# Kernel tuning notes

Hardware: AMD Instinct MI355X
Metric: run time of the kernel (lower is better)

Reference implementation:

```python
import jax, jax.numpy as jnp
import numpy as np

B, N, D, H = 8, 8192, 512, 8  # batch, seq, hidden, heads
DH = D // H


def _rope_tables(n, d, dtype=jnp.float32):
    # standard rotate-half RoPE tables over the full hidden dim (d/2 freq pairs)
    half = d // 2
    inv_freq = 1.0 / (10000.0 ** (np.arange(0, half, dtype=np.float32) / half))
    pos = np.arange(n, dtype=np.float32)
    ang = np.einsum('n,f->nf', pos, inv_freq)          # [N, D/2]
    ang = np.concatenate([ang, ang], axis=-1)          # [N, D]
    return jnp.asarray(np.cos(ang), dtype), jnp.asarray(np.sin(ang), dtype)


def setup_inputs() -> dict:
    key = jax.random.key(0)
    k1, k2 = jax.random.split(key)
    hidden_states = jax.random.normal(k1, (B, N, D), dtype=jnp.float32)
    num_layers = 24
    std = 0.02 / np.sqrt(2.0 * num_layers * D)
    W = jax.random.normal(k2, (D, D), dtype=jnp.float32) * std
    cos, sin = _rope_tables(N, D)
    return {"hidden_states": hidden_states, "W": W, "cos": cos, "sin": sin}


def _rotate_half(x):
    x1, x2 = jnp.split(x, 2, axis=-1)
    return jnp.concatenate([-x2, x1], axis=-1)


def reference(hidden_states, W, cos, sin):
    # dropout(p=0) in eval mode -> identity
    x = hidden_states * cos + _rotate_half(hidden_states) * sin  # RoPE, [B,N,D]
    q = jnp.einsum('bnd,ed->bne', x, W)                          # F.linear(x, W)
    qh = q.reshape(B, N, H, DH)
    xh = x.reshape(B, N, H, DH)
    # linear-complexity path: (K^T V) then Q @ (.), per head
    kv = jnp.einsum('bnhd,bnhe->bhde', xh, xh)   # [B,H,DH,DH]
    out = jnp.einsum('bnhd,bhde->bnhe', qh, kv)  # [B,N,H,DH]
    return out.reshape(B, N, D)
```

## Files before the change

### kernel.cpp

```cpp
#include <hip/hip_runtime.h>
#include <hip/hip_bf16.h>
#include <stdint.h>

#define BB 8
#define NN 8192
#define DD 512
#define HH 8
#define DHD 64
#define NCH 16

typedef __attribute__((ext_vector_type(8))) short bf16x8;
typedef __attribute__((ext_vector_type(4))) float f32x4;
typedef __attribute__((ext_vector_type(4))) float f4v;

__device__ __forceinline__ unsigned short f2bf(float f) {
  union { float f; unsigned int u; } v; v.f = f;
  return (unsigned short)((v.u + 0x7FFFu + ((v.u >> 16) & 1u)) >> 16);
}

__device__ __forceinline__ void async16(const void* g, void* l) {
  __builtin_amdgcn_global_load_lds(
      (const __attribute__((address_space(1))) void*)g,
      (__attribute__((address_space(3))) void*)l, 16, 0, 0);
}

__global__ void rope_kernel(const float* __restrict__ h, const float* __restrict__ cs,
                            const float* __restrict__ sn, unsigned short* __restrict__ x) {
  int t = blockIdx.x * 256 + threadIdx.x;
  int r = t >> 6;
  int c = (t & 63) << 2;
  int n = r & (NN - 1);
  size_t base  = (size_t)r * DD + c;
  size_t tbase = (size_t)n * DD + c;
  f4v h1 = __builtin_nontemporal_load((const f4v*)(h + base));
  f4v h2 = __builtin_nontemporal_load((const f4v*)(h + base + 256));
  f4v c1 = *(const f4v*)(cs + tbase);
  f4v c2 = *(const f4v*)(cs + tbase + 256);
  f4v s1 = *(const f4v*)(sn + tbase);
  f4v s2 = *(const f4v*)(sn + tbase + 256);
  f4v x1 = h1 * c1 - h2 * s1;
  f4v x2 = h2 * c2 + h1 * s2;
  uint2 p1, p2;
  p1.x = (unsigned)f2bf(x1.x) | ((unsigned)f2bf(x1.y) << 16);
  p1.y = (unsigned)f2bf(x1.z) | ((unsigned)f2bf(x1.w) << 16);
  p2.x = (unsigned)f2bf(x2.x) | ((unsigned)f2bf(x2.y) << 16);
  p2.y = (unsigned)f2bf(x2.z) | ((unsigned)f2bf(x2.w) << 16);
  *(uint2*)(x + base)       = p1;
  *(uint2*)(x + base + 256) = p2;
}

__global__ void kv_kernel(const unsigned short* __restrict__ x, float* __restrict__ kvp) {
  __shared__ __align__(16) unsigned short xt[64 * 68];
  int bh = blockIdx.x;
  int b = bh >> 3, hh = bh & 7;
  int chunk = blockIdx.y;
  int tid = threadIdx.x;
  int wave = tid >> 6, lane = tid & 63;
  int d0 = (wave & 1) * 32, e0 = (wave >> 1) * 32;
  int l15 = lane & 15, q = lane >> 4;
  f32x4 acc[2][2];
#pragma unroll
  for (int i = 0; i < 2; ++i)
#pragma unroll
    for (int j = 0; j < 2; ++j) acc[i][j] = (f32x4){0.f, 0.f, 0.f, 0.f};

  int rp  = tid & 31;
  int seg = tid >> 5;
  const unsigned short* srcbase = x + (size_t)b * NN * DD + hh * DHD + seg * 8;

  for (int t = 0; t < 8; ++t) {
    int n0 = chunk * 512 + t * 64;
    const unsigned short* s0 = srcbase + (size_t)(n0 + 2 * rp) * DD;
    uint4 p0 = *(const uint4*)(s0);
    uint4 p1 = *(const uint4*)(s0 + DD);
    unsigned short a0[8], a1[8];
    *(uint4*)a0 = p0;  *(uint4*)a1 = p1;
    __syncthreads();
#pragma unroll
    for (int j = 0; j < 8; ++j) {
      unsigned pack = (unsigned)a0[j] | ((unsigned)a1[j] << 16);
      ((unsigned*)xt)[(seg * 8 + j) * 34 + rp] = pack;
    }
    __syncthreads();
#pragma unroll
    for (int ks = 0; ks < 64; ks += 32) {
      bf16x8 a0f = *(const bf16x8*)&xt[(d0 + l15) * 68 + ks + q * 8];
      bf16x8 a1f = *(const bf16x8*)&xt[(d0 + 16 + l15) * 68 + ks + q * 8];
      bf16x8 b0f = *(const bf16x8*)&xt[(e0 + l15) * 68 + ks + q * 8];
      bf16x8 b1f = *(const bf16x8*)&xt[(e0 + 16 + l15) * 68 + ks + q * 8];
      acc[0][0] = __builtin_amdgcn_mfma_f32_16x16x32_bf16(a0f, b0f, acc[0][0], 0, 0, 0);
      acc[1][0] = __builtin_amdgcn_mfma_f32_16x16x32_bf16(a1f, b0f, acc[1][0], 0, 0, 0);
      acc[0][1] = __builtin_amdgcn_mfma_f32_16x16x32_bf16(a0f, b1f, acc[0][1], 0, 0, 0);
      acc[1][1] = __builtin_amdgcn_mfma_f32_16x16x32_bf16(a1f, b1f, acc[1][1], 0, 0, 0);
    }
  }
  float* dst = kvp + ((size_t)chunk * gridDim.x + bh) * 4096;
#pragma unroll
  for (int i = 0; i < 2; ++i)
#pragma unroll
    for (int j = 0; j < 2; ++j) {
      int col = e0 + j * 16 + l15;
#pragma unroll
      for (int reg = 0; reg < 4; ++reg) {
        int row = d0 + i * 16 + q * 4 + reg;
        dst[row * 64 + col] = acc[i][j][reg];
      }
    }
}

__global__ void wkvt_kernel(const float* __restrict__ W, const float* __restrict__ kvp,
                            unsigned short* __restrict__ wkvt) {
  __shared__ float kvs[4096];
  __shared__ float ws[8192];
  int bh = blockIdx.x, fc = blockIdx.y;
  int nbh = gridDim.x;
  int b = bh >> 3, hh = bh & 7;
  int f0 = fc * 128;
  int tid = threadIdx.x;
#pragma unroll
  for (int i = 0; i < 4; ++i) {
    int idx = i * 1024 + tid * 4;
    f4v s = (f4v){0.f, 0.f, 0.f, 0.f};
    for (int c = 0; c < NCH; ++c)
      s += *(const f4v*)&kvp[((size_t)c * nbh + bh) * 4096 + idx];
    *(f4v*)&kvs[idx] = s;
  }
#pragma unroll
  for (int i = 0; i < 8; ++i) {
    int idx = i * 1024 + tid * 4;
    int d = idx >> 7, f = idx & 127;
    *(float4*)&ws[idx] = *(const float4*)&W[(size_t)(hh * DHD + d) * DD + f0 + f];
  }
  __syncthreads();
  int e = tid & 63, fg = tid >> 6;
  float acc[32];
#pragma unroll
  for (int j = 0; j < 32; ++j) acc[j] = 0.f;
  for (int d = 0; d < 64; ++d) {
    float kvv = kvs[d * 64 + e];
    const float* wr = &ws[d * 128 + fg * 32];
#pragma unroll
    for (int j = 0; j < 32; ++j) acc[j] = fmaf(wr[j], kvv, acc[j]);
  }
  unsigned short tmp[32];
#pragma unroll
  for (int j = 0; j < 32; ++j) tmp[j] = f2bf(acc[j]);
  size_t obase = ((size_t)(b * DD + hh * DHD + e)) * DD + f0 + fg * 32;
#pragma unroll
  for (int qq = 0; qq < 4; ++qq)
    *(uint4*)&wkvt[obase + qq * 8] = *(uint4*)&tmp[qq * 8];
}

__global__ __launch_bounds__(256, 2) void gemm_kernel(const unsigned short* __restrict__ x,
                                                      const unsigned short* __restrict__ wkvt,
                                                      float* __restrict__ out) {
  __shared__ __align__(16) unsigned short As[128 * 64];
  __shared__ __align__(16) unsigned short Bs[256 * 64];
  int mt = blockIdx.x, ct = blockIdx.y, bz = blockIdx.z;
  int tid = threadIdx.x, wave = tid >> 6, lane = tid & 63;
  int m_off = (wave & 1) * 64, c_off = (wave >> 1) * 128;
  int l15 = lane & 15, q = lane >> 4;
  int lrow = lane >> 3, lcol = (lane & 7) * 8;
  const unsigned short* Ag = x    + ((size_t)bz * NN + mt * 128) * DD;
  const unsigned short* Bg = wkvt + ((size_t)bz * DD + ct * 256) * DD;
  f32x4 acc[4][8];
#pragma unroll
  for (int i = 0; i < 4; ++i)
#pragma unroll
    for (int j = 0; j < 8; ++j) acc[i][j] = (f32x4){0.f, 0.f, 0.f, 0.f};

  for (int kk = 0; kk < 512; kk += 64) {
#pragma unroll
    for (int i = 0; i < 4; ++i)
      async16(Ag + (size_t)(wave * 32 + i * 8 + lrow) * DD + kk + lcol,
              &As[(wave * 32 + i * 8) * 64]);
#pragma unroll
    for (int i = 0; i < 8; ++i)
      async16(Bg + (size_t)(wave * 64 + i * 8 + lrow) * DD + kk + lcol,
              &Bs[(wave * 64 + i * 8) * 64]);
    __syncthreads();
#pragma unroll
    for (int ks = 0; ks < 64; ks += 32) {
      bf16x8 a[4], bb[8];
#pragma unroll
      for (int i = 0; i < 4; ++i)
        a[i] = *(const bf16x8*)&As[(m_off + i * 16 + l15) * 64 + ks + q * 8];
#pragma unroll
      for (int j = 0; j < 8; ++j)
        bb[j] = *(const bf16x8*)&Bs[(c_off + j * 16 + l15) * 64 + ks + q * 8];
#pragma unroll
      for (int i = 0; i < 4; ++i)
#pragma unroll
        for (int j = 0; j < 8; ++j)
          acc[i][j] = __builtin_amdgcn_mfma_f32_16x16x32_bf16(a[i], bb[j], acc[i][j], 0, 0, 0);
    }
    __syncthreads();
  }
  float* ob = out + ((size_t)bz * NN + mt * 128) * DD + ct * 256;
#pragma unroll
  for (int i = 0; i < 4; ++i)
#pragma unroll
    for (int j = 0; j < 8; ++j) {
      int row = m_off + i * 16 + q * 4;
      int col = c_off + j * 16 + l15;
#pragma unroll
      for (int reg = 0; reg < 4; ++reg)
        ob[(size_t)(row + reg) * DD + col] = acc[i][j][reg];
    }
}

extern "C" void kernel_launch(void* const* d_in, const int* in_sizes, int n_in,
                              void* d_out, int out_size, void* d_ws, size_t ws_size,
                              hipStream_t stream) {
  (void)in_sizes; (void)n_in; (void)out_size;
  const float* h  = (const float*)d_in[0];
  const float* W  = (const float*)d_in[1];
  const float* cs = (const float*)d_in[2];
  const float* sn = (const float*)d_in[3];
  float* out = (float*)d_out;

  const size_t x_full     = (size_t)BB * NN * DD * 2;
  const size_t kvp_full   = (size_t)NCH * BB * HH * DHD * DHD * 4;
  const size_t wkvt_full  = (size_t)BB * DD * DD * 2;
  const size_t x_batch    = (size_t)NN * DD * 2;
  const size_t kvp_batch  = (size_t)NCH * HH * DHD * DHD * 4;
  const size_t wkvt_batch = (size_t)DD * DD * 2;

  if (ws_size >= x_full + kvp_full + wkvt_full) {
    unsigned short* xw   = (unsigned short*)d_ws;
    float*          kvp  = (float*)((char*)d_ws + x_full);
    unsigned short* wkvt = (unsigned short*)((char*)d_ws + x_full + kvp_full);
    rope_kernel<<<dim3(BB * NN * 64 / 256), dim3(256), 0, stream>>>(h, cs, sn, xw);
    kv_kernel<<<dim3(BB * HH, NCH), dim3(256), 0, stream>>>(xw, kvp);
    wkvt_kernel<<<dim3(BB * HH, 4), dim3(256), 0, stream>>>(W, kvp, wkvt);
    gemm_kernel<<<dim3(NN / 128, DD / 256, BB), dim3(256), 0, stream>>>(xw, wkvt, out);
  } else {
    unsigned short* xw   = (unsigned short*)d_ws;
    float*          kvp  = (float*)((char*)d_ws + x_batch);
    unsigned short* wkvt = (unsigned short*)((char*)d_ws + x_batch + kvp_batch);
    for (int b = 0; b < BB; ++b) {
      rope_kernel<<<dim3(NN * 64 / 256), dim3(256), 0, stream>>>(
          h + (size_t)b * NN * DD, cs, sn, xw);
      kv_kernel<<<dim3(HH, NCH), dim3(256), 0, stream>>>(xw, kvp);
      wkvt_kernel<<<dim3(HH, 4), dim3(256), 0, stream>>>(W, kvp, wkvt);
      gemm_kernel<<<dim3(NN / 128, DD / 256, 1), dim3(256), 0, stream>>>(
          xw, wkvt, out + (size_t)b * NN * DD);
    }
  }
}
```

Before: 335.4 us.

## Fuse RoPE into KV reduction kernel and restructure W·KV product

Merges the RoPE kernel with the per-head K^T V accumulation: each 512-thread block applies RoPE to 256 rows, writes the bf16 x for the later GEMM, and transposes the result into LDS to compute all 8 heads' 64x64 KV partials with MFMA, prefetching the next tile's inputs. This removes the separate launch and the re-read of x from global memory. The wkvt kernel is reshaped to load all of W's head rows per block with vectorized FMAs over 16 output columns, and the GEMM output uses nontemporal stores. The trade-off is only 256 blocks for the fused kernel, which may underfill the GPU, and more partial chunks to reduce.

```diff
diff --git a/kernel.cpp b/kernel.cpp
--- a/kernel.cpp
+++ b/kernel.cpp
@@ -7,7 +7,7 @@
 #define DD 512
 #define HH 8
 #define DHD 64
-#define NCH 16
+#define NCH 32
 
 typedef __attribute__((ext_vector_type(8))) short bf16x8;
 typedef __attribute__((ext_vector_type(4))) float f32x4;
@@ -24,131 +24,170 @@
       (__attribute__((address_space(3))) void*)l, 16, 0, 0);
 }
 
-__global__ void rope_kernel(const float* __restrict__ h, const float* __restrict__ cs,
-                            const float* __restrict__ sn, unsigned short* __restrict__ x) {
-  int t = blockIdx.x * 256 + threadIdx.x;
-  int r = t >> 6;
-  int c = (t & 63) << 2;
-  int n = r & (NN - 1);
-  size_t base  = (size_t)r * DD + c;
-  size_t tbase = (size_t)n * DD + c;
-  f4v h1 = __builtin_nontemporal_load((const f4v*)(h + base));
-  f4v h2 = __builtin_nontemporal_load((const f4v*)(h + base + 256));
-  f4v c1 = *(const f4v*)(cs + tbase);
-  f4v c2 = *(const f4v*)(cs + tbase + 256);
-  f4v s1 = *(const f4v*)(sn + tbase);
-  f4v s2 = *(const f4v*)(sn + tbase + 256);
-  f4v x1 = h1 * c1 - h2 * s1;
-  f4v x2 = h2 * c2 + h1 * s2;
-  uint2 p1, p2;
-  p1.x = (unsigned)f2bf(x1.x) | ((unsigned)f2bf(x1.y) << 16);
-  p1.y = (unsigned)f2bf(x1.z) | ((unsigned)f2bf(x1.w) << 16);
-  p2.x = (unsigned)f2bf(x2.x) | ((unsigned)f2bf(x2.y) << 16);
-  p2.y = (unsigned)f2bf(x2.z) | ((unsigned)f2bf(x2.w) << 16);
-  *(uint2*)(x + base)       = p1;
-  *(uint2*)(x + base + 256) = p2;
-}
-
-__global__ void kv_kernel(const unsigned short* __restrict__ x, float* __restrict__ kvp) {
-  __shared__ __align__(16) unsigned short xt[64 * 68];
-  int bh = blockIdx.x;
-  int b = bh >> 3, hh = bh & 7;
-  int chunk = blockIdx.y;
+__global__ __launch_bounds__(512, 2) void ropekv_kernel(
+    const float* __restrict__ h, const float* __restrict__ cs,
+    const float* __restrict__ sn, unsigned short* __restrict__ x,
+    float* __restrict__ kvp, int nbh) {
+  __shared__ __align__(16) unsigned int xt32[512 * 34];
+  int blk = blockIdx.x;
+  int chunk = blk & 31, b = blk >> 5;
   int tid = threadIdx.x;
   int wave = tid >> 6, lane = tid & 63;
-  int d0 = (wave & 1) * 32, e0 = (wave >> 1) * 32;
+  int rpar = lane & 1;
+  int g = lane >> 1;
+  int cf = g * 8;
   int l15 = lane & 15, q = lane >> 4;
-  f32x4 acc[2][2];
-#pragma unroll
-  for (int i = 0; i < 2; ++i)
-#pragma unroll
-    for (int j = 0; j < 2; ++j) acc[i][j] = (f32x4){0.f, 0.f, 0.f, 0.f};
-
-  int rp  = tid & 31;
-  int seg = tid >> 5;
-  const unsigned short* srcbase = x + (size_t)b * NN * DD + hh * DHD + seg * 8;
-
-  for (int t = 0; t < 8; ++t) {
-    int n0 = chunk * 512 + t * 64;
-    const unsigned short* s0 = srcbase + (size_t)(n0 + 2 * rp) * DD;
-    uint4 p0 = *(const uint4*)(s0);
-    uint4 p1 = *(const uint4*)(s0 + DD);
-    unsigned short a0[8], a1[8];
-    *(uint4*)a0 = p0;  *(uint4*)a1 = p1;
-    __syncthreads();
-#pragma unroll
-    for (int j = 0; j < 8; ++j) {
-      unsigned pack = (unsigned)a0[j] | ((unsigned)a1[j] << 16);
-      ((unsigned*)xt)[(seg * 8 + j) * 34 + rp] = pack;
-    }
-    __syncthreads();
+  int hd = wave * 64;
+  size_t row0 = (size_t)b * NN + (size_t)chunk * 256;
+  int n0 = chunk * 256;
+
+  f32x4 acc[4][4];
+#pragma unroll
+  for (int i = 0; i < 4; ++i)
+#pragma unroll
+    for (int j = 0; j < 4; ++j) acc[i][j] = (f32x4){0.f, 0.f, 0.f, 0.f};
+
+  f4v ha[4][2], hbv[4][2];
+
+  auto loadt = [&](int t) {
+#pragma unroll
+    for (int p = 0; p < 4; ++p) {
+      int r = p * 16 + wave * 2 + rpar;
+      const float* hp = h + (row0 + t * 64 + r) * DD + cf;
+      ha[p][0]  = __builtin_nontemporal_load((const f4v*)hp);
+      ha[p][1]  = __builtin_nontemporal_load((const f4v*)(hp + 4));
+      hbv[p][0] = __builtin_nontemporal_load((const f4v*)(hp + 256));
+      hbv[p][1] = __builtin_nontemporal_load((const f4v*)(hp + 260));
+    }
+  };
+
+  auto ropet = [&](int t) {
+#pragma unroll
+    for (int p = 0; p < 4; ++p) {
+      int r = p * 16 + wave * 2 + rpar;
+      int nr = n0 + t * 64 + r;
+      const float* cp = cs + (size_t)nr * DD + cf;
+      const float* sp = sn + (size_t)nr * DD + cf;
+      f4v c0 = *(const f4v*)cp, c1 = *(const f4v*)(cp + 4);
+      f4v s0 = *(const f4v*)sp, s1 = *(const f4v*)(sp + 4);
+      f4v xl0 = ha[p][0] * c0 - hbv[p][0] * s0;
+      f4v xl1 = ha[p][1] * c1 - hbv[p][1] * s1;
+      f4v xh0 = hbv[p][0] * c0 + ha[p][0] * s0;
+      f4v xh1 = hbv[p][1] * c1 + ha[p][1] * s1;
+      unsigned ml[4], mh[4];
+      ml[0] = (unsigned)f2bf(xl0.x) | ((unsigned)f2bf(xl0.y) << 16);
+      ml[1] = (unsigned)f2bf(xl0.z) | ((unsigned)f2bf(xl0.w) << 16);
+      ml[2] = (unsigned)f2bf(xl1.x) | ((unsigned)f2bf(xl1.y) << 16);
+      ml[3] = (unsigned)f2bf(xl1.z) | ((unsigned)f2bf(xl1.w) << 16);
+      mh[0] = (unsigned)f2bf(xh0.x) | ((unsigned)f2bf(xh0.y) << 16);
+      mh[1] = (unsigned)f2bf(xh0.z) | ((unsigned)f2bf(xh0.w) << 16);
+      mh[2] = (unsigned)f2bf(xh1.x) | ((unsigned)f2bf(xh1.y) << 16);
+      mh[3] = (unsigned)f2bf(xh1.z) | ((unsigned)f2bf(xh1.w) << 16);
+      unsigned short* xp = x + (row0 + t * 64 + r) * DD + cf;
+      uint4 st0; st0.x = ml[0]; st0.y = ml[1]; st0.z = ml[2]; st0.w = ml[3];
+      uint4 st1; st1.x = mh[0]; st1.y = mh[1]; st1.z = mh[2]; st1.w = mh[3];
+      *(uint4*)xp         = st0;
+      *(uint4*)(xp + 256) = st1;
+      unsigned pk[8];
+#pragma unroll
+      for (int k = 0; k < 4; ++k) {
+        unsigned mine = rpar ? mh[k] : ml[k];
+        unsigned send = rpar ? ml[k] : mh[k];
+        unsigned recv = (unsigned)__shfl_xor((int)send, 1, 64);
+        if (!rpar) {
+          pk[2 * k]     = (mine & 0xffffu) | (recv << 16);
+          pk[2 * k + 1] = (mine >> 16) | (recv & 0xffff0000u);
+        } else {
+          pk[2 * k]     = (recv & 0xffffu) | (mine << 16);
+          pk[2 * k + 1] = (recv >> 16) | (mine & 0xffff0000u);
+        }
+      }
+      int np = p * 8 + wave;
+      int dbase = cf + (rpar ? 256 : 0);
+      int rot = (g >> 1) & 7;
+#pragma unroll
+      for (int w = 0; w < 8; ++w) {
+        int jj = (w + rot) & 7;
+        xt32[(dbase + jj) * 34 + np] = pk[jj];
+      }
+    }
+  };
+
+  loadt(0);
+  for (int t = 0; t < 4; ++t) {
+    ropet(t);
+    __syncthreads();
+    if (t < 3) loadt(t + 1);
+    const unsigned short* xt16 = (const unsigned short*)xt32;
 #pragma unroll
     for (int ks = 0; ks < 64; ks += 32) {
-      bf16x8 a0f = *(const bf16x8*)&xt[(d0 + l15) * 68 + ks + q * 8];
-      bf16x8 a1f = *(const bf16x8*)&xt[(d0 + 16 + l15) * 68 + ks + q * 8];
-      bf16x8 b0f = *(const bf16x8*)&xt[(e0 + l15) * 68 + ks + q * 8];
-      bf16x8 b1f = *(const bf16x8*)&xt[(e0 + 16 + l15) * 68 + ks + q * 8];
-      acc[0][0] = __builtin_amdgcn_mfma_f32_16x16x32_bf16(a0f, b0f, acc[0][0], 0, 0, 0);
-      acc[1][0] = __builtin_amdgcn_mfma_f32_16x16x32_bf16(a1f, b0f, acc[1][0], 0, 0, 0);
-      acc[0][1] = __builtin_amdgcn_mfma_f32_16x16x32_bf16(a0f, b1f, acc[0][1], 0, 0, 0);
-      acc[1][1] = __builtin_amdgcn_mfma_f32_16x16x32_bf16(a1f, b1f, acc[1][1], 0, 0, 0);
-    }
-  }
-  float* dst = kvp + ((size_t)chunk * gridDim.x + bh) * 4096;
-#pragma unroll
-  for (int i = 0; i < 2; ++i)
-#pragma unroll
-    for (int j = 0; j < 2; ++j) {
-      int col = e0 + j * 16 + l15;
-#pragma unroll
-      for (int reg = 0; reg < 4; ++reg) {
-        int row = d0 + i * 16 + q * 4 + reg;
-        dst[row * 64 + col] = acc[i][j][reg];
-      }
-    }
-}
-
-__global__ void wkvt_kernel(const float* __restrict__ W, const float* __restrict__ kvp,
-                            unsigned short* __restrict__ wkvt) {
-  __shared__ float kvs[4096];
-  __shared__ float ws[8192];
-  int bh = blockIdx.x, fc = blockIdx.y;
-  int nbh = gridDim.x;
+      bf16x8 af[4];
+#pragma unroll
+      for (int i = 0; i < 4; ++i)
+        af[i] = *(const bf16x8*)&xt16[(hd + i * 16 + l15) * 68 + ks + q * 8];
+#pragma unroll
+      for (int i = 0; i < 4; ++i)
+#pragma unroll
+        for (int j = 0; j < 4; ++j)
+          acc[i][j] = __builtin_amdgcn_mfma_f32_16x16x32_bf16(af[i], af[j], acc[i][j], 0, 0, 0);
+    }
+    __syncthreads();
+  }
+
+  int bh = b * 8 + wave;
+  float* dst = kvp + ((size_t)chunk * nbh + bh) * 4096;
+#pragma unroll
+  for (int i = 0; i < 4; ++i)
+#pragma unroll
+    for (int j = 0; j < 4; ++j)
+#pragma unroll
+      for (int reg = 0; reg < 4; ++reg)
+        dst[(i * 16 + q * 4 + reg) * 64 + j * 16 + l15] = acc[i][j][reg];
+}
+
+__global__ __launch_bounds__(512, 2) void wkvt_kernel(
+    const float* __restrict__ W, const float* __restrict__ kvp,
+    unsigned short* __restrict__ wkvt, int nbh) {
+  __shared__ float kvs[64 * 16];
+  __shared__ __align__(16) float ws[64 * 512];
+  int blk = blockIdx.x;
+  int bh = blk >> 2, eq = blk & 3;
   int b = bh >> 3, hh = bh & 7;
-  int f0 = fc * 128;
   int tid = threadIdx.x;
-#pragma unroll
-  for (int i = 0; i < 4; ++i) {
-    int idx = i * 1024 + tid * 4;
+  if (tid < 256) {
+    int idx = tid * 4;
+    int d = idx >> 4, ec = idx & 15;
     f4v s = (f4v){0.f, 0.f, 0.f, 0.f};
     for (int c = 0; c < NCH; ++c)
-      s += *(const f4v*)&kvp[((size_t)c * nbh + bh) * 4096 + idx];
+      s += *(const f4v*)&kvp[((size_t)c * nbh + bh) * 4096 + d * 64 + eq * 16 + ec];
     *(f4v*)&kvs[idx] = s;
   }
 #pragma unroll
-  for (int i = 0; i < 8; ++i) {
-    int idx = i * 1024 + tid * 4;
-    int d = idx >> 7, f = idx & 127;
-    *(float4*)&ws[idx] = *(const float4*)&W[(size_t)(hh * DHD + d) * DD + f0 + f];
+  for (int i = 0; i < 16; ++i) {
+    int idx = i * 2048 + tid * 4;
+    *(f4v*)&ws[idx] = *(const f4v*)&W[(size_t)(hh * DHD + (idx >> 9)) * DD + (idx & 511)];
   }
   __syncthreads();
-  int e = tid & 63, fg = tid >> 6;
-  float acc[32];
-#pragma unroll
-  for (int j = 0; j < 32; ++j) acc[j] = 0.f;
+  int el = tid & 15, fg = tid >> 4;
+  f4v av[4];
+#pragma unroll
+  for (int k = 0; k < 4; ++k) av[k] = (f4v){0.f, 0.f, 0.f, 0.f};
+#pragma unroll 8
   for (int d = 0; d < 64; ++d) {
-    float kvv = kvs[d * 64 + e];
-    const float* wr = &ws[d * 128 + fg * 32];
-#pragma unroll
-    for (int j = 0; j < 32; ++j) acc[j] = fmaf(wr[j], kvv, acc[j]);
-  }
-  unsigned short tmp[32];
-#pragma unroll
-  for (int j = 0; j < 32; ++j) tmp[j] = f2bf(acc[j]);
-  size_t obase = ((size_t)(b * DD + hh * DHD + e)) * DD + f0 + fg * 32;
-#pragma unroll
-  for (int qq = 0; qq < 4; ++qq)
-    *(uint4*)&wkvt[obase + qq * 8] = *(uint4*)&tmp[qq * 8];
+    float kvv = kvs[d * 16 + el];
+    const f4v* wr = (const f4v*)&ws[d * DD + fg * 16];
+#pragma unroll
+    for (int k = 0; k < 4; ++k) av[k] += wr[k] * kvv;
+  }
+  unsigned short tb[16];
+#pragma unroll
+  for (int k = 0; k < 4; ++k) {
+    tb[k * 4 + 0] = f2bf(av[k].x); tb[k * 4 + 1] = f2bf(av[k].y);
+    tb[k * 4 + 2] = f2bf(av[k].z); tb[k * 4 + 3] = f2bf(av[k].w);
+  }
+  size_t ob = ((size_t)b * DD + hh * DHD + eq * 16 + el) * DD + fg * 16;
+  *(uint4*)&wkvt[ob]     = *(uint4*)&tb[0];
+  *(uint4*)&wkvt[ob + 8] = *(uint4*)&tb[8];
 }
 
 __global__ __launch_bounds__(256, 2) void gemm_kernel(const unsigned short* __restrict__ x,
@@ -205,7 +244,7 @@
       int col = c_off + j * 16 + l15;
 #pragma unroll
       for (int reg = 0; reg < 4; ++reg)
-        ob[(size_t)(row + reg) * DD + col] = acc[i][j][reg];
+        __builtin_nontemporal_store(acc[i][j][reg], &ob[(size_t)(row + reg) * DD + col]);
     }
 }
 
@@ -230,19 +269,17 @@
     unsigned short* xw   = (unsigned short*)d_ws;
     float*          kvp  = (float*)((char*)d_ws + x_full);
     unsigned short* wkvt = (unsigned short*)((char*)d_ws + x_full + kvp_full);
-    rope_kernel<<<dim3(BB * NN * 64 / 256), dim3(256), 0, stream>>>(h, cs, sn, xw);
-    kv_kernel<<<dim3(BB * HH, NCH), dim3(256), 0, stream>>>(xw, kvp);
-    wkvt_kernel<<<dim3(BB * HH, 4), dim3(256), 0, stream>>>(W, kvp, wkvt);
+    ropekv_kernel<<<dim3(BB * 32), dim3(512), 0, stream>>>(h, cs, sn, xw, kvp, BB * HH);
+    wkvt_kernel<<<dim3(BB * HH * 4), dim3(512), 0, stream>>>(W, kvp, wkvt, BB * HH);
     gemm_kernel<<<dim3(NN / 128, DD / 256, BB), dim3(256), 0, stream>>>(xw, wkvt, out);
   } else {
     unsigned short* xw   = (unsigned short*)d_ws;
     float*          kvp  = (float*)((char*)d_ws + x_batch);
     unsigned short* wkvt = (unsigned short*)((char*)d_ws + x_batch + kvp_batch);
     for (int b = 0; b < BB; ++b) {
-      rope_kernel<<<dim3(NN * 64 / 256), dim3(256), 0, stream>>>(
-          h + (size_t)b * NN * DD, cs, sn, xw);
-      kv_kernel<<<dim3(HH, NCH), dim3(256), 0, stream>>>(xw, kvp);
-      wkvt_kernel<<<dim3(HH, 4), dim3(256), 0, stream>>>(W, kvp, wkvt);
+      ropekv_kernel<<<dim3(32), dim3(512), 0, stream>>>(
+          h + (size_t)b * NN * DD, cs, sn, xw, kvp, HH);
+      wkvt_kernel<<<dim3(HH * 4), dim3(512), 0, stream>>>(W, kvp, wkvt, HH);
       gemm_kernel<<<dim3(NN / 128, DD / 256, 1), dim3(256), 0, stream>>>(
           xw, wkvt, out + (size_t)b * NN * DD);
     }
```

Measured after the change: 336.0 us. Within noise of the previous version (+0.2%).
